# Kernel optimization log

Measured on AMD Instinct MI355X. Metric: run time of the kernel, lower is better.

The kernel has to match this reference:

```python
import jax, jax.numpy as jnp
import numpy as np

N_NODES = 50000


def _gcn_conv(x, W, b, src, dst, norm, n_nodes):
    # x: [N, Fin], W: [Fin, Fout]
    h = x @ W                                   # [N, Fout]
    msg = h[src] * norm[:, None]                # [E+N, Fout] edge messages
    out = jax.ops.segment_sum(msg, dst, num_segments=n_nodes)
    return out + b


def reference(x, edge_index, W1, b1, W2, b2):
    n = x.shape[0]
    # add self-loops (PyG GCNConv default add_self_loops=True)
    loop = jnp.arange(n, dtype=edge_index.dtype)
    src = jnp.concatenate([edge_index[0], loop])
    dst = jnp.concatenate([edge_index[1], loop])
    # symmetric degree normalization: deg over destination with unit weights
    deg = jax.ops.segment_sum(jnp.ones_like(dst, dtype=x.dtype), dst, num_segments=n)
    dinv = jnp.where(deg > 0, jax.lax.rsqrt(deg), 0.0)
    norm = dinv[src] * dinv[dst]                # [E+N]
    h = _gcn_conv(x, W1, b1, src, dst, norm, n)
    h = jax.nn.relu(h)
    out = _gcn_conv(h, W2, b2, src, dst, norm, n)
    return out


def setup_inputs() -> dict:
    key = jax.random.key(0)
    k1, k2, k3, k4 = jax.random.split(key, 4)
    n, e, fin, hid, fout = N_NODES, 800000, 128, 128, 64
    x = jax.random.normal(k1, (n, fin), dtype=jnp.float32)
    edge_index = jax.random.randint(k2, (2, e), 0, n, dtype=jnp.int64)
    # Glorot-ish init for linear weights, zero bias (PyG default)
    W1 = jax.random.normal(k3, (fin, hid), dtype=jnp.float32) / np.sqrt(fin)
    b1 = jnp.zeros((hid,), dtype=jnp.float32)
    W2 = jax.random.normal(k4, (hid, fout), dtype=jnp.float32) / np.sqrt(hid)
    b2 = jnp.zeros((fout,), dtype=jnp.float32)
    return {"x": x, "edge_index": edge_index, "W1": W1, "b1": b1, "W2": W2, "b2": b2}
```

## Files before the change

### kernel.cpp

```cpp
#include <hip/hip_runtime.h>
#include <hip/hip_bf16.h>


constexpr int FIN = 128;
constexpr int HID = 128;
constexpr int FOUT = 64;
constexpr int CAP = 48;
constexpr int NPB = 98;
constexpr int BCAP = 3072;
constexpr int OVF_MAX = 65536;

typedef __attribute__((ext_vector_type(8))) short s16x8;
typedef __attribute__((ext_vector_type(4))) float f32x4;

static __device__ __forceinline__ float bf2f(__hip_bfloat16 v) { return __bfloat162float(v); }
static __device__ __forceinline__ float lo2f(unsigned u) { union { unsigned i; float f; } c; c.i = u << 16; return c.f; }
static __device__ __forceinline__ float hi2f(unsigned u) { union { unsigned i; float f; } c; c.i = u & 0xffff0000u; return c.f; }
static __device__ __forceinline__ unsigned short f2bfu(float f) {
    __hip_bfloat16 h = __float2bfloat16(f);
    union { __hip_bfloat16 h; unsigned short u; } c; c.h = h; return c.u;
}
static __device__ __forceinline__ unsigned pack2(float a, float b) {
    return (unsigned)f2bfu(a) | ((unsigned)f2bfu(b) << 16);
}
static __device__ __forceinline__ void acc_add(float* acc, uint4 v) {
    acc[0] += lo2f(v.x); acc[1] += hi2f(v.x);
    acc[2] += lo2f(v.y); acc[3] += hi2f(v.y);
    acc[4] += lo2f(v.z); acc[5] += hi2f(v.z);
    acc[6] += lo2f(v.w); acc[7] += hi2f(v.w);
}

__global__ __launch_bounds__(256) void k_detect(const unsigned* __restrict__ xw,
                                                const int* __restrict__ eiw,
                                                int E, int* __restrict__ flags,
                                                int* __restrict__ gcur,
                                                int* __restrict__ cnt, int N) {
    for (long i = (long)blockIdx.x * 256 + threadIdx.x; i < N; i += (long)gridDim.x * 256)
        cnt[i] = 0;
    if (blockIdx.x != 0) return;
    for (int i = threadIdx.x; i < 514; i += 256) gcur[i] = 0;
    __shared__ int s_bf16like, s_oddnz;
    if (threadIdx.x == 0) { s_bf16like = 0; s_oddnz = 0; }
    __syncthreads();
    int c = 0;
    for (int i = threadIdx.x; i < 4096; i += 256) {
        unsigned ex = ((xw[i] & 0xffffu) >> 7) & 0xffu;
        if (ex >= 117u && ex <= 130u) c++;
    }
    atomicAdd(&s_bf16like, c);
    int nz = 0;
    for (int i = threadIdx.x; i < 2048; i += 256)
        if (eiw[2 * i + 1] != 0) nz++;
    atomicAdd(&s_oddnz, nz);
    __syncthreads();
    if (threadIdx.x == 0) {
        flags[0] = (s_bf16like < 2048) ? 1 : 0;
        flags[1] = (s_oddnz == 0) ? 1 : 0;
    }
}

__global__ __launch_bounds__(256) void k_binA(const int* __restrict__ ei, int E, int N,
                                              int nbuk,
                                              int* __restrict__ gcur,
                                              unsigned* __restrict__ pairs,
                                              int2* __restrict__ ovfA,
                                              int* __restrict__ ovfAcnt,
                                              const int* __restrict__ flags) {
    __shared__ int hist[512];
    __shared__ int gbase[512];
    const int tid = threadIdx.x;
    const long base = (long)blockIdx.x * 2048;
    const bool i64 = flags[1] != 0;
    int se[8], de[8];
    for (int b = tid; b < nbuk; b += 256) hist[b] = 0;
    __syncthreads();
#pragma unroll
    for (int j = 0; j < 8; ++j) {
        long i = base + j * 256 + tid;
        int s = 0, d = -1;
        if (i < E) {
            if (i64) { s = ((const int2*)ei)[i].x; d = ((const int2*)(ei + 2 * (long)E))[i].x; }
            else     { s = ei[i]; d = ei[(long)E + i]; }
            if ((unsigned)s >= (unsigned)N || (unsigned)d >= (unsigned)N) d = -1;
        }
        se[j] = s; de[j] = d;
        if (d >= 0) atomicAdd(&hist[d / NPB], 1);
    }
    __syncthreads();
    for (int b = tid; b < nbuk; b += 256) {
        int h = hist[b];
        gbase[b] = h > 0 ? atomicAdd(&gcur[b], h) : 0;
        hist[b] = 0;
    }
    __syncthreads();
#pragma unroll
    for (int j = 0; j < 8; ++j) {
        int d = de[j];
        if (d < 0) continue;
        int b = d / NPB;
        int p = gbase[b] + atomicAdd(&hist[b], 1);
        if (p < BCAP) {
            pairs[(long)b * BCAP + p] = ((unsigned)(d - b * NPB) << 16) | (unsigned)se[j];
        } else {
            int op = atomicAdd(ovfAcnt, 1);
            if (op < OVF_MAX) ovfA[op] = make_int2(d, se[j]);
        }
    }
}

__global__ __launch_bounds__(256) void k_binB(const int* __restrict__ gcur,
                                              const unsigned* __restrict__ pairs,
                                              int* __restrict__ cnt,
                                              unsigned short* __restrict__ slots,
                                              int2* __restrict__ ovf2,
                                              int* __restrict__ ovf2cnt, int N) {
    __shared__ int cntL[NPB];
    __shared__ __align__(16) unsigned short slotsL[NPB * CAP];
    const int b = blockIdx.x;
    const int tid = threadIdx.x;
    const int d0 = b * NPB;
    const int nd = min(NPB, N - d0);
    if (nd <= 0) return;
    for (int i = tid; i < NPB; i += 256) cntL[i] = 0;
    __syncthreads();
    const int c = min(gcur[b], BCAP);
    const unsigned* pb = pairs + (long)b * BCAP;
    for (int i = tid; i < c; i += 256) {
        unsigned p = pb[i];
        int ld = p >> 16;
        int pos = atomicAdd(&cntL[ld], 1);
        if (pos < CAP) {
            slotsL[ld * CAP + pos] = (unsigned short)(p & 0xffffu);
        } else {
            int op = atomicAdd(ovf2cnt, 1);
            if (op < OVF_MAX) ovf2[op] = make_int2(d0 + ld, (int)(p & 0xffffu));
        }
    }
    __syncthreads();
    for (int i = tid; i < nd; i += 256) cnt[d0 + i] = cntL[i];
    const uint4* sv = (const uint4*)slotsL;
    uint4* gv = (uint4*)(slots + (long)d0 * CAP);
    const int total8 = (nd * CAP) >> 3;
    for (int i = tid; i < total8; i += 256) gv[i] = sv[i];
}

template<typename ST>
__global__ __launch_bounds__(256) void k_patch(const int2* __restrict__ ovfA,
                                               const int* __restrict__ ovfAcnt,
                                               int* __restrict__ cnt,
                                               ST* __restrict__ slots,
                                               int2* __restrict__ ovf2,
                                               int* __restrict__ ovf2cnt, int N) {
    int n = *ovfAcnt; n = n < OVF_MAX ? n : OVF_MAX;
    for (int i = blockIdx.x * 256 + threadIdx.x; i < n; i += gridDim.x * 256) {
        int2 p = ovfA[i];
        int pos = atomicAdd(&cnt[p.x], 1);
        if (pos < CAP) {
            slots[(long)p.x * CAP + pos] = (ST)p.y;
        } else {
            int op = atomicAdd(ovf2cnt, 1);
            if (op < OVF_MAX) ovf2[op] = p;
        }
    }
}

__global__ __launch_bounds__(256) void k_build_direct(const int* __restrict__ ei, int E, int N,
                                                      int* __restrict__ cnt,
                                                      int* __restrict__ slots,
                                                      int2* __restrict__ ovf2,
                                                      int* __restrict__ ovf2cnt,
                                                      const int* __restrict__ flags) {
    long i = (long)blockIdx.x * 256 + threadIdx.x;
    if (i >= E) return;
    int s, d;
    if (flags[1]) { s = ((const int2*)ei)[i].x; d = ((const int2*)(ei + 2 * (long)E))[i].x; }
    else          { s = ei[i]; d = ei[(long)E + i]; }
    if ((unsigned)s >= (unsigned)N || (unsigned)d >= (unsigned)N) return;
    int pos = atomicAdd(&cnt[d], 1);
    if (pos < CAP) {
        slots[(long)d * CAP + pos] = s;
    } else {
        int op = atomicAdd(ovf2cnt, 1);
        if (op < OVF_MAX) ovf2[op] = make_int2(d, s);
    }
}

template<int CT>
__global__ __launch_bounds__(256) void k_gemm(const void* __restrict__ Xp, int x_follows_flag,
                                              const void* __restrict__ Wp,
                                              const int* __restrict__ cnt,
                                              __hip_bfloat16* __restrict__ G,
                                              const int* __restrict__ flags, int N) {
    constexpr int C = CT * 16;
    __shared__ __align__(16) short Wt[C * 136];
    const bool f32m = flags[0] != 0;
    const bool xf32 = (x_follows_flag != 0) && f32m;
    const int tid = threadIdx.x;
    for (int i = tid; i < 128 * C; i += 256) {
        int k = i / C, n = i % C;
        float wv = f32m ? ((const float*)Wp)[(long)k * C + n]
                        : bf2f(((const __hip_bfloat16*)Wp)[(long)k * C + n]);
        Wt[n * 136 + k] = (short)f2bfu(wv);
    }
    __syncthreads();
    const int w = tid >> 6, lane = tid & 63;
    const int m = lane & 15, quad = lane >> 4;
    const int rowA = blockIdx.x * 64 + w * 16 + m;
    const int rowc = rowA < N ? rowA : N - 1;
    s16x8 afr[4];
#pragma unroll
    for (int kc = 0; kc < 4; ++kc) {
        const int k0 = kc * 32 + quad * 8;
        if (!xf32) {
            afr[kc] = *(const s16x8*)((const __hip_bfloat16*)Xp + (long)rowc * 128 + k0);
        } else {
            const float* p = (const float*)Xp + (long)rowc * 128 + k0;
            s16x8 t;
#pragma unroll
            for (int j = 0; j < 8; ++j) t[j] = (short)f2bfu(p[j]);
            afr[kc] = t;
        }
    }
    const int rbase = blockIdx.x * 64 + w * 16 + quad * 4;
    float dv[4];
#pragma unroll
    for (int r = 0; r < 4; ++r) {
        int rr = min(rbase + r, N - 1);
        dv[r] = rsqrtf((float)(cnt[rr] + 1));
    }
#pragma unroll
    for (int ct = 0; ct < CT; ++ct) {
        f32x4 acc = {0.f, 0.f, 0.f, 0.f};
#pragma unroll
        for (int kc = 0; kc < 4; ++kc) {
            s16x8 bfr = *(const s16x8*)&Wt[(ct * 16 + m) * 136 + kc * 32 + quad * 8];
            acc = __builtin_amdgcn_mfma_f32_16x16x32_bf16(afr[kc], bfr, acc, 0, 0, 0);
        }
#pragma unroll
        for (int r = 0; r < 4; ++r) {
            int rr = rbase + r;
            if (rr < N) G[(long)rr * C + ct * 16 + m] = __float2bfloat16(dv[r] * acc[r]);
        }
    }
}

template<int F, int LAYER1, typename ST>
__global__ __launch_bounds__(256) void k_gather(const __hip_bfloat16* __restrict__ G,
                                                const int* __restrict__ cnt,
                                                const ST* __restrict__ slots,
                                                const int2* __restrict__ ovf2,
                                                const int* __restrict__ ovf2cnt,
                                                const void* __restrict__ bias,
                                                void* __restrict__ outp,
                                                const int* __restrict__ flags, int N) {
    constexpr int L = F / 8;
    constexpr int NODES = 256 / L;
    const int tid = threadIdx.x;
    const int grp = tid / L, lane = tid % L;
    const int node = blockIdx.x * NODES + grp;
    if (node >= N) return;
    const int cd = cnt[node];
    const float wself = rsqrtf((float)(cd + 1));
    const int m = cd < CAP ? cd : CAP;
    const ST* sl = slots + (long)node * CAP;
    float acc[8] = {0, 0, 0, 0, 0, 0, 0, 0};
    acc_add(acc, ((const uint4*)(G + (long)node * F))[lane]);
    int i = 0;
    for (; i + 7 < m; i += 8) {
        int s0 = sl[i], s1 = sl[i + 1], s2 = sl[i + 2], s3 = sl[i + 3];
        int s4 = sl[i + 4], s5 = sl[i + 5], s6 = sl[i + 6], s7 = sl[i + 7];
        uint4 v0 = ((const uint4*)(G + (long)s0 * F))[lane];
        uint4 v1 = ((const uint4*)(G + (long)s1 * F))[lane];
        uint4 v2 = ((const uint4*)(G + (long)s2 * F))[lane];
        uint4 v3 = ((const uint4*)(G + (long)s3 * F))[lane];
        uint4 v4 = ((const uint4*)(G + (long)s4 * F))[lane];
        uint4 v5 = ((const uint4*)(G + (long)s5 * F))[lane];
        uint4 v6 = ((const uint4*)(G + (long)s6 * F))[lane];
        uint4 v7 = ((const uint4*)(G + (long)s7 * F))[lane];
        acc_add(acc, v0); acc_add(acc, v1); acc_add(acc, v2); acc_add(acc, v3);
        acc_add(acc, v4); acc_add(acc, v5); acc_add(acc, v6); acc_add(acc, v7);
    }
    for (; i + 3 < m; i += 4) {
        int s0 = sl[i], s1 = sl[i + 1], s2 = sl[i + 2], s3 = sl[i + 3];
        uint4 v0 = ((const uint4*)(G + (long)s0 * F))[lane];
        uint4 v1 = ((const uint4*)(G + (long)s1 * F))[lane];
        uint4 v2 = ((const uint4*)(G + (long)s2 * F))[lane];
        uint4 v3 = ((const uint4*)(G + (long)s3 * F))[lane];
        acc_add(acc, v0); acc_add(acc, v1); acc_add(acc, v2); acc_add(acc, v3);
    }
    for (; i < m; ++i)
        acc_add(acc, ((const uint4*)(G + (long)sl[i] * F))[lane]);
    if (cd > CAP) {
        int oc = *ovf2cnt; oc = oc < OVF_MAX ? oc : OVF_MAX;
        for (int j = 0; j < oc; ++j)
            if (ovf2[j].x == node)
                acc_add(acc, ((const uint4*)(G + (long)ovf2[j].y * F))[lane]);
    }
    const bool f32m = flags[0] != 0;
    const int c0 = lane * 8;
    float bv[8];
    if (f32m) {
        const float4* bp = (const float4*)((const float*)bias + c0);
        float4 b0 = bp[0], b1 = bp[1];
        bv[0] = b0.x; bv[1] = b0.y; bv[2] = b0.z; bv[3] = b0.w;
        bv[4] = b1.x; bv[5] = b1.y; bv[6] = b1.z; bv[7] = b1.w;
    } else {
        uint4 b = *(const uint4*)((const __hip_bfloat16*)bias + c0);
        bv[0] = lo2f(b.x); bv[1] = hi2f(b.x); bv[2] = lo2f(b.y); bv[3] = hi2f(b.y);
        bv[4] = lo2f(b.z); bv[5] = hi2f(b.z); bv[6] = lo2f(b.w); bv[7] = hi2f(b.w);
    }
    float o[8];
#pragma unroll
    for (int c = 0; c < 8; ++c) {
        float v = wself * acc[c] + bv[c];
        o[c] = (LAYER1 && v < 0.f) ? 0.f : v;
    }
    if (LAYER1 || !f32m) {
        uint4 pv = { pack2(o[0], o[1]), pack2(o[2], o[3]), pack2(o[4], o[5]), pack2(o[6], o[7]) };
        ((uint4*)outp)[(long)node * L + lane] = pv;
    } else {
        float4* op = (float4*)((float*)outp + (long)node * F + c0);
        op[0] = make_float4(o[0], o[1], o[2], o[3]);
        op[1] = make_float4(o[4], o[5], o[6], o[7]);
    }
}

extern "C" void kernel_launch(void* const* d_in, const int* in_sizes, int n_in,
                              void* d_out, int out_size, void* d_ws, size_t ws_size,
                              hipStream_t stream) {
    const void* x  = d_in[0];
    const int*  ei = (const int*)d_in[1];
    const void* W1 = d_in[2];
    const void* b1 = d_in[3];
    const void* W2 = d_in[4];
    const void* b2 = d_in[5];

    const int N = in_sizes[0] / FIN;
    const int E = in_sizes[1] / 2;
    const int nbuk = (N + NPB - 1) / NPB;

    char* ws = (char*)d_ws;
    int*   flags   = (int*)ws;
    int*   gcur    = (int*)(ws + 4096);
    int*   ovfAcnt = gcur + 512;
    int*   ovf2cnt = gcur + 513;
    int*   cnt     = (int*)(ws + 65536);
    int2*  ovfA    = (int2*)(ws + 524288);
    int2*  ovf2    = (int2*)(ws + 1048576);
    unsigned short* slots16 = (unsigned short*)(ws + 2097152);
    int*   slots32 = (int*)(ws + 2097152);
    __hip_bfloat16* g  = (__hip_bfloat16*)(ws + 11730944);
    __hip_bfloat16* g2 = g;
    unsigned* pairs = (unsigned*)(ws + 24530944);
    __hip_bfloat16* h1 = (__hip_bfloat16*)(ws + 24530944);

    const int GB = (N + 63) / 64;
    const int AB = (E + 2047) / 2048;
    const int EB = (E + 255) / 256;

    k_detect<<<64, 256, 0, stream>>>((const unsigned*)x, ei, E, flags, gcur, cnt, N);

    if (N <= 65536 && nbuk <= 512) {
        k_binA<<<AB, 256, 0, stream>>>(ei, E, N, nbuk, gcur, pairs, ovfA, ovfAcnt, flags);
        k_binB<<<nbuk, 256, 0, stream>>>(gcur, pairs, cnt, slots16, ovf2, ovf2cnt, N);
        k_patch<unsigned short><<<32, 256, 0, stream>>>(ovfA, ovfAcnt, cnt, slots16, ovf2, ovf2cnt, N);
        k_gemm<8><<<GB, 256, 0, stream>>>(x, 1, W1, cnt, g, flags, N);
        k_gather<128, 1, unsigned short><<<(N + 15) / 16, 256, 0, stream>>>(
            g, cnt, slots16, ovf2, ovf2cnt, b1, h1, flags, N);
        k_gemm<4><<<GB, 256, 0, stream>>>(h1, 0, W2, cnt, g2, flags, N);
        k_gather<64, 0, unsigned short><<<(N + 31) / 32, 256, 0, stream>>>(
            g2, cnt, slots16, ovf2, ovf2cnt, b2, d_out, flags, N);
    } else {
        k_build_direct<<<EB, 256, 0, stream>>>(ei, E, N, cnt, slots32, ovf2, ovf2cnt, flags);
        k_gemm<8><<<GB, 256, 0, stream>>>(x, 1, W1, cnt, g, flags, N);
        k_gather<128, 1, int><<<(N + 15) / 16, 256, 0, stream>>>(
            g, cnt, slots32, ovf2, ovf2cnt, b1, h1, flags, N);
        k_gemm<4><<<GB, 256, 0, stream>>>(h1, 0, W2, cnt, g2, flags, N);
        k_gather<64, 0, int><<<(N + 31) / 32, 256, 0, stream>>>(
            g2, cnt, slots32, ovf2, ovf2cnt, b2, d_out, flags, N);
    }
}
```

Measured before the change: 208.7 us.

## Split layer-1 features into two column planes and fold overflow patch into binB

The layer-1 GEMM now writes its output as two 64-column planes, and the layer-1 gather runs as two passes, one per plane. Each pass gathers 128-byte rows, which shrinks the random-access working set and should fit the cache better. The overflow patch kernel is removed: every binB block now scans the global overflow list and inserts its own entries into shared memory, which saves one launch. The cost is a second gather pass that rereads the slots and counts, and every bucket block scanning the whole overflow list.

```diff
diff --git a/kernel.cpp b/kernel.cpp
--- a/kernel.cpp
+++ b/kernel.cpp
@@ -110,6 +110,8 @@
 
 __global__ __launch_bounds__(256) void k_binB(const int* __restrict__ gcur,
                                               const unsigned* __restrict__ pairs,
+                                              const int2* __restrict__ ovfA,
+                                              const int* __restrict__ ovfAcnt,
                                               int* __restrict__ cnt,
                                               unsigned short* __restrict__ slots,
                                               int2* __restrict__ ovf2,
@@ -136,32 +138,26 @@
             if (op < OVF_MAX) ovf2[op] = make_int2(d0 + ld, (int)(p & 0xffffu));
         }
     }
+    int na = *ovfAcnt; na = na < OVF_MAX ? na : OVF_MAX;
+    for (int i = tid; i < na; i += 256) {
+        int2 p = ovfA[i];
+        int ld = p.x - d0;
+        if ((unsigned)ld < (unsigned)nd) {
+            int pos = atomicAdd(&cntL[ld], 1);
+            if (pos < CAP) {
+                slotsL[ld * CAP + pos] = (unsigned short)p.y;
+            } else {
+                int op = atomicAdd(ovf2cnt, 1);
+                if (op < OVF_MAX) ovf2[op] = p;
+            }
+        }
+    }
     __syncthreads();
     for (int i = tid; i < nd; i += 256) cnt[d0 + i] = cntL[i];
     const uint4* sv = (const uint4*)slotsL;
     uint4* gv = (uint4*)(slots + (long)d0 * CAP);
     const int total8 = (nd * CAP) >> 3;
     for (int i = tid; i < total8; i += 256) gv[i] = sv[i];
-}
-
-template<typename ST>
-__global__ __launch_bounds__(256) void k_patch(const int2* __restrict__ ovfA,
-                                               const int* __restrict__ ovfAcnt,
-                                               int* __restrict__ cnt,
-                                               ST* __restrict__ slots,
-                                               int2* __restrict__ ovf2,
-                                               int* __restrict__ ovf2cnt, int N) {
-    int n = *ovfAcnt; n = n < OVF_MAX ? n : OVF_MAX;
-    for (int i = blockIdx.x * 256 + threadIdx.x; i < n; i += gridDim.x * 256) {
-        int2 p = ovfA[i];
-        int pos = atomicAdd(&cnt[p.x], 1);
-        if (pos < CAP) {
-            slots[(long)p.x * CAP + pos] = (ST)p.y;
-        } else {
-            int op = atomicAdd(ovf2cnt, 1);
-            if (op < OVF_MAX) ovf2[op] = p;
-        }
-    }
 }
 
 __global__ __launch_bounds__(256) void k_build_direct(const int* __restrict__ ei, int E, int N,
@@ -185,7 +181,7 @@
     }
 }
 
-template<int CT>
+template<int CT, int SPLIT>
 __global__ __launch_bounds__(256) void k_gemm(const void* __restrict__ Xp, int x_follows_flag,
                                               const void* __restrict__ Wp,
                                               const int* __restrict__ cnt,
@@ -239,9 +235,92 @@
 #pragma unroll
         for (int r = 0; r < 4; ++r) {
             int rr = rbase + r;
-            if (rr < N) G[(long)rr * C + ct * 16 + m] = __float2bfloat16(dv[r] * acc[r]);
-        }
-    }
+            if (rr < N) {
+                long off;
+                if (SPLIT) {
+                    const int plane = ct / (CT / 2);
+                    const int cp = (ct % (CT / 2)) * 16 + m;
+                    off = (long)plane * N * (C / 2) + (long)rr * (C / 2) + cp;
+                } else {
+                    off = (long)rr * C + ct * 16 + m;
+                }
+                G[off] = __float2bfloat16(dv[r] * acc[r]);
+            }
+        }
+    }
+}
+
+__global__ __launch_bounds__(256) void k_gather_half(const __hip_bfloat16* __restrict__ Gp,
+                                                     const int* __restrict__ cnt,
+                                                     const unsigned short* __restrict__ slots,
+                                                     const int2* __restrict__ ovf2,
+                                                     const int* __restrict__ ovf2cnt,
+                                                     const void* __restrict__ b1,
+                                                     __hip_bfloat16* __restrict__ h1,
+                                                     const int* __restrict__ flags,
+                                                     int N, int P) {
+    const int tid = threadIdx.x;
+    const int grp = tid >> 3, lane = tid & 7;
+    const int node = blockIdx.x * 32 + grp;
+    if (node >= N) return;
+    const int cd = cnt[node];
+    const float wself = rsqrtf((float)(cd + 1));
+    const int m = cd < CAP ? cd : CAP;
+    const unsigned short* sl = slots + (long)node * CAP;
+    float acc[8] = {0, 0, 0, 0, 0, 0, 0, 0};
+    acc_add(acc, ((const uint4*)(Gp + (long)node * 64))[lane]);
+    int i = 0;
+    for (; i + 7 < m; i += 8) {
+        int s0 = sl[i], s1 = sl[i + 1], s2 = sl[i + 2], s3 = sl[i + 3];
+        int s4 = sl[i + 4], s5 = sl[i + 5], s6 = sl[i + 6], s7 = sl[i + 7];
+        uint4 v0 = ((const uint4*)(Gp + (long)s0 * 64))[lane];
+        uint4 v1 = ((const uint4*)(Gp + (long)s1 * 64))[lane];
+        uint4 v2 = ((const uint4*)(Gp + (long)s2 * 64))[lane];
+        uint4 v3 = ((const uint4*)(Gp + (long)s3 * 64))[lane];
+        uint4 v4 = ((const uint4*)(Gp + (long)s4 * 64))[lane];
+        uint4 v5 = ((const uint4*)(Gp + (long)s5 * 64))[lane];
+        uint4 v6 = ((const uint4*)(Gp + (long)s6 * 64))[lane];
+        uint4 v7 = ((const uint4*)(Gp + (long)s7 * 64))[lane];
+        acc_add(acc, v0); acc_add(acc, v1); acc_add(acc, v2); acc_add(acc, v3);
+        acc_add(acc, v4); acc_add(acc, v5); acc_add(acc, v6); acc_add(acc, v7);
+    }
+    for (; i + 3 < m; i += 4) {
+        int s0 = sl[i], s1 = sl[i + 1], s2 = sl[i + 2], s3 = sl[i + 3];
+        uint4 v0 = ((const uint4*)(Gp + (long)s0 * 64))[lane];
+        uint4 v1 = ((const uint4*)(Gp + (long)s1 * 64))[lane];
+        uint4 v2 = ((const uint4*)(Gp + (long)s2 * 64))[lane];
+        uint4 v3 = ((const uint4*)(Gp + (long)s3 * 64))[lane];
+        acc_add(acc, v0); acc_add(acc, v1); acc_add(acc, v2); acc_add(acc, v3);
+    }
+    for (; i < m; ++i)
+        acc_add(acc, ((const uint4*)(Gp + (long)sl[i] * 64))[lane]);
+    if (cd > CAP) {
+        int oc = *ovf2cnt; oc = oc < OVF_MAX ? oc : OVF_MAX;
+        for (int j = 0; j < oc; ++j)
+            if (ovf2[j].x == node)
+                acc_add(acc, ((const uint4*)(Gp + (long)ovf2[j].y * 64))[lane]);
+    }
+    const bool f32m = flags[0] != 0;
+    const int c0 = P * 64 + lane * 8;
+    float bv[8];
+    if (f32m) {
+        const float4* bp = (const float4*)((const float*)b1 + c0);
+        float4 b0 = bp[0], b1v = bp[1];
+        bv[0] = b0.x; bv[1] = b0.y; bv[2] = b0.z; bv[3] = b0.w;
+        bv[4] = b1v.x; bv[5] = b1v.y; bv[6] = b1v.z; bv[7] = b1v.w;
+    } else {
+        uint4 b = *(const uint4*)((const __hip_bfloat16*)b1 + c0);
+        bv[0] = lo2f(b.x); bv[1] = hi2f(b.x); bv[2] = lo2f(b.y); bv[3] = hi2f(b.y);
+        bv[4] = lo2f(b.z); bv[5] = hi2f(b.z); bv[6] = lo2f(b.w); bv[7] = hi2f(b.w);
+    }
+    float o[8];
+#pragma unroll
+    for (int c = 0; c < 8; ++c) {
+        float v = wself * acc[c] + bv[c];
+        o[c] = v > 0.f ? v : 0.f;
+    }
+    uint4 pv = { pack2(o[0], o[1]), pack2(o[2], o[3]), pack2(o[4], o[5]), pack2(o[6], o[7]) };
+    ((uint4*)(h1 + (long)node * 128 + P * 64))[lane] = pv;
 }
 
 template<int F, int LAYER1, typename ST>
@@ -362,20 +441,19 @@
 
     if (N <= 65536 && nbuk <= 512) {
         k_binA<<<AB, 256, 0, stream>>>(ei, E, N, nbuk, gcur, pairs, ovfA, ovfAcnt, flags);
-        k_binB<<<nbuk, 256, 0, stream>>>(gcur, pairs, cnt, slots16, ovf2, ovf2cnt, N);
-        k_patch<unsigned short><<<32, 256, 0, stream>>>(ovfA, ovfAcnt, cnt, slots16, ovf2, ovf2cnt, N);
-        k_gemm<8><<<GB, 256, 0, stream>>>(x, 1, W1, cnt, g, flags, N);
-        k_gather<128, 1, unsigned short><<<(N + 15) / 16, 256, 0, stream>>>(
-            g, cnt, slots16, ovf2, ovf2cnt, b1, h1, flags, N);
-        k_gemm<4><<<GB, 256, 0, stream>>>(h1, 0, W2, cnt, g2, flags, N);
+        k_binB<<<nbuk, 256, 0, stream>>>(gcur, pairs, ovfA, ovfAcnt, cnt, slots16, ovf2, ovf2cnt, N);
+        k_gemm<8, 1><<<GB, 256, 0, stream>>>(x, 1, W1, cnt, g, flags, N);
+        k_gather_half<<<(N + 31) / 32, 256, 0, stream>>>(g, cnt, slots16, ovf2, ovf2cnt, b1, h1, flags, N, 0);
+        k_gather_half<<<(N + 31) / 32, 256, 0, stream>>>(g + (long)N * 64, cnt, slots16, ovf2, ovf2cnt, b1, h1, flags, N, 1);
+        k_gemm<4, 0><<<GB, 256, 0, stream>>>(h1, 0, W2, cnt, g2, flags, N);
         k_gather<64, 0, unsigned short><<<(N + 31) / 32, 256, 0, stream>>>(
             g2, cnt, slots16, ovf2, ovf2cnt, b2, d_out, flags, N);
     } else {
         k_build_direct<<<EB, 256, 0, stream>>>(ei, E, N, cnt, slots32, ovf2, ovf2cnt, flags);
-        k_gemm<8><<<GB, 256, 0, stream>>>(x, 1, W1, cnt, g, flags, N);
+        k_gemm<8, 0><<<GB, 256, 0, stream>>>(x, 1, W1, cnt, g, flags, N);
         k_gather<128, 1, int><<<(N + 15) / 16, 256, 0, stream>>>(
             g, cnt, slots32, ovf2, ovf2cnt, b1, h1, flags, N);
-        k_gemm<4><<<GB, 256, 0, stream>>>(h1, 0, W2, cnt, g2, flags, N);
+        k_gemm<4, 0><<<GB, 256, 0, stream>>>(h1, 0, W2, cnt, g2, flags, N);
         k_gather<64, 0, int><<<(N + 31) / 32, 256, 0, stream>>>(
             g2, cnt, slots32, ovf2, ovf2cnt, b2, d_out, flags, N);
     }
```

Result: faster. 202.7 us (-2.9%).
